# Kernel optimization log

Measured on AMD Instinct MI355X. Metric: run time of the kernel, lower is better.

The kernel has to match this reference:

```python
import jax, jax.numpy as jnp
import numpy as np

N = 50000
HID = 128
NH = 4
E_RES, E_SEQ, E_KNN = 100000, 100000, 200000
BN_EPS = 1e-5
NEG_SLOPE = 0.2


def _gat(h, src, dst, W, al, ar, resW, b):
    """DGL-style GATConv (eval mode: feat_drop off, residual=True, bias).
    h: (N, in), W/resW: (in, H*out), al/ar: (H, out), b: (H*out,)"""
    Hh, out = al.shape
    feat = (h @ W).reshape(N, Hh, out)                 # (N, H, out)
    el = jnp.sum(feat * al, axis=-1)                   # (N, H)
    er = jnp.sum(feat * ar, axis=-1)                   # (N, H)
    e = jax.nn.leaky_relu(el[src] + er[dst], NEG_SLOPE)  # (E, H)
    # edge softmax over incoming edges of each dst node (numerically stable)
    m = jax.ops.segment_max(e, dst, num_segments=N)    # (N, H)
    ex = jnp.exp(e - m[dst])
    s = jax.ops.segment_sum(ex, dst, num_segments=N)
    a = ex / s[dst]                                    # (E, H)
    msg = a[:, :, None] * feat[src]                    # (E, H, out)
    rst = jax.ops.segment_sum(msg, dst, num_segments=N)  # (N, H, out)
    return rst + (h @ resW).reshape(N, Hh, out) + b.reshape(1, Hh, out)


def _hetero(h, src_res, dst_res, src_seq, dst_seq, src_knn, dst_knn, W, al, ar, resW, b):
    # HeteroGraphConv with aggregate='sum' over relations, then mean over heads
    r = _gat(h, src_res, dst_res, W[0], al[0], ar[0], resW[0], b[0])
    r = r + _gat(h, src_seq, dst_seq, W[1], al[1], ar[1], resW[1], b[1])
    r = r + _gat(h, src_knn, dst_knn, W[2], al[2], ar[2], resW[2], b[2])
    return jnp.mean(r, axis=1)                         # (N, out)


def setup_inputs() -> dict:
    key = jax.random.key(0)
    ks = iter(jax.random.split(key, 32))
    inp = {}
    inp["x"] = jax.random.normal(next(ks), (N, HID), jnp.float32)
    inp["src_res"] = jax.random.randint(next(ks), (E_RES,), 0, N, jnp.int32)
    inp["dst_res"] = jax.random.randint(next(ks), (E_RES,), 0, N, jnp.int32)
    inp["src_seq"] = jax.random.randint(next(ks), (E_SEQ,), 0, N, jnp.int32)
    inp["dst_seq"] = jax.random.randint(next(ks), (E_SEQ,), 0, N, jnp.int32)
    inp["src_knn"] = jax.random.randint(next(ks), (E_KNN,), 0, N, jnp.int32)
    inp["dst_knn"] = jax.random.randint(next(ks), (E_KNN,), 0, N, jnp.int32)
    sc = 0.05
    for l in (0, 1):
        inp[f"W{l}"] = jax.random.normal(next(ks), (3, HID, NH * HID), jnp.float32) * sc
        inp[f"al{l}"] = jax.random.normal(next(ks), (3, NH, HID), jnp.float32) * sc
        inp[f"ar{l}"] = jax.random.normal(next(ks), (3, NH, HID), jnp.float32) * sc
        inp[f"resW{l}"] = jax.random.normal(next(ks), (3, HID, NH * HID), jnp.float32) * sc
        inp[f"b{l}"] = jax.random.normal(next(ks), (3, NH * HID), jnp.float32) * sc
    inp["fc_W"] = jax.random.normal(next(ks), (HID, HID), jnp.float32) * sc
    inp["fc_b"] = jax.random.normal(next(ks), (HID,), jnp.float32) * sc
    inp["bn_gamma"] = jnp.ones((HID,), jnp.float32)
    inp["bn_beta"] = jnp.zeros((HID,), jnp.float32)
    inp["bn_mean"] = jax.random.normal(next(ks), (HID,), jnp.float32) * sc
    inp["bn_var"] = jax.random.uniform(next(ks), (HID,), jnp.float32)
    return inp


def reference(x, src_res, dst_res, src_seq, dst_seq, src_knn, dst_knn,
              W0, al0, ar0, resW0, b0, W1, al1, ar1, resW1, b1,
              fc_W, fc_b, bn_gamma, bn_beta, bn_mean, bn_var):
    # layer 0: hetero GAT, head-mean, fc + ReLU + BatchNorm (eval), dropout=identity
    h = _hetero(x, src_res, dst_res, src_seq, dst_seq, src_knn, dst_knn,
                W0, al0, ar0, resW0, b0)
    h = jax.nn.relu(h @ fc_W + fc_b)
    h = (h - bn_mean) / jnp.sqrt(bn_var + BN_EPS) * bn_gamma + bn_beta
    # layer 1 (final): hetero GAT, head-mean
    out = _hetero(h, src_res, dst_res, src_seq, dst_seq, src_knn, dst_knn,
                  W1, al1, ar1, resW1, b1)
    return out
```

## Files before the change

kernel.cpp:

```cpp
#include <hip/hip_runtime.h>
#include <hip/hip_bf16.h>
#include <math.h>
#include <stdint.h>

#define NNODES 50000
#define SCHUNK 4096
#define AW 1664
#define XOFF 1536

typedef __bf16 bf16x8 __attribute__((ext_vector_type(8)));
typedef float f32x4 __attribute__((ext_vector_type(4)));
typedef unsigned short u16;
typedef unsigned int u32;

__device__ __forceinline__ float lrelu(float x){ return x >= 0.f ? x : 0.2f*x; }
__device__ __forceinline__ float b2f(u16 u){ union{ u32 i; float f; } c; c.i = ((u32)u)<<16; return c.f; }
__device__ __forceinline__ float lo2f(u32 v){ union{ u32 i; float f; } c; c.i = v<<16; return c.f; }
__device__ __forceinline__ float hi2f(u32 v){ union{ u32 i; float f; } c; c.i = v & 0xffff0000u; return c.f; }
__device__ __forceinline__ u16 f2b(float f){ __hip_bfloat16 h = __float2bfloat16(f); return *(u16*)&h; }
__device__ __forceinline__ u32 packbf(float a, float b){ return (u32)f2b(a) | ((u32)f2b(b) << 16); }

#define GLDS16(g, l) __builtin_amdgcn_global_load_lds( \
    (const __attribute__((address_space(1))) void*)(g), \
    (__attribute__((address_space(3))) void*)(l), 16, 0, 0)

__global__ void prep_b(const float* __restrict__ W0, const float* __restrict__ W1,
                       const float* __restrict__ resW0, const float* __restrict__ resW1,
                       const float* __restrict__ b0, const float* __restrict__ b1,
                       u16* __restrict__ Btb, float* __restrict__ biasf)
{
    int gid = blockIdx.x*blockDim.x + threadIdx.x;
    if (gid < 2*128*AW){
        int l = gid / (128*AW);
        int rem = gid - l*(128*AW);
        int c = rem / AW;
        int j = rem - c*AW;
        const float* W  = l ? W1 : W0;
        const float* rw = l ? resW1 : resW0;
        float v;
        if (j < XOFF){
            int r = j >> 9, h = (j >> 7) & 3, k = j & 127;
            v = 0.25f * W[(size_t)r*65536 + (size_t)k*512 + h*128 + c];
        } else {
            int k = j - XOFF;
            float s = 0.f;
            for (int r = 0; r < 3; ++r)
                for (int h = 0; h < 4; ++h)
                    s += rw[(size_t)r*65536 + (size_t)k*512 + h*128 + c];
            v = 0.25f * s;
        }
        Btb[gid] = f2b(v);
    }
    if (gid < 256){
        int l = gid >> 7, c = gid & 127;
        const float* bb = l ? b1 : b0;
        float s = 0.f;
        for (int r = 0; r < 3; ++r)
            for (int h = 0; h < 4; ++h)
                s += bb[r*512 + h*128 + c];
        biasf[gid] = 0.25f*s;
    }
}

__global__ void prep_wl(const float* __restrict__ W0, const float* __restrict__ W1,
                        const float* __restrict__ al0, const float* __restrict__ ar0,
                        const float* __restrict__ al1, const float* __restrict__ ar1,
                        const float* __restrict__ fcW,
                        u16* __restrict__ wlb, u16* __restrict__ fcWtb)
{
    int gid = blockIdx.x*blockDim.x + threadIdx.x;
    if (gid < 2*128*128){
        int l = gid >> 14;
        int col = (gid >> 7) & 127;
        int k = gid & 127;
        float v = 0.f;
        if (col < 24){
            int r = col >> 3, lr = (col >> 2) & 1, h = col & 3;
            const float* W = l ? W1 : W0;
            const float* av = l ? (lr ? ar1 : al1) : (lr ? ar0 : al0);
            const float* wrow = W + (size_t)r*65536 + (size_t)k*512 + h*128;
            const float* arow = av + r*512 + h*128;
            for (int cc = 0; cc < 128; ++cc) v += wrow[cc]*arow[cc];
        }
        wlb[gid] = f2b(v);
    }
    if (gid < 128*128){
        int k = gid & 127, n = gid >> 7;
        fcWtb[gid] = f2b(fcW[k*128 + n]);
    }
}

__global__ __launch_bounds__(256) void xprep_kernel(const float* __restrict__ x,
    u16* __restrict__ Ax, const u16* __restrict__ wl, float* __restrict__ el, int M)
{
    __shared__ u16 Xs[64*136];
    __shared__ u16 Ws[32*136];
    const int tid = threadIdx.x;
    const int row0 = blockIdx.x*64;
    #pragma unroll
    for (int p = 0; p < 2; ++p){
        int idx = tid + p*256;
        int c = idx >> 4, kc = (idx & 15)*8;
        float4 v = make_float4(0.f,0.f,0.f,0.f);
        if (c < 24) v = *(const float4*)(wl + c*128 + kc);
        *(float4*)&Ws[c*136 + kc] = v;
    }
    int r = tid >> 2, cq = (tid & 3)*32;
    int grow = row0 + r;
    if (grow < M){
        #pragma unroll
        for (int i = 0; i < 8; ++i){
            float4 v = *(const float4*)(x + (size_t)grow*128 + cq + i*4);
            ushort4 o;
            o.x = f2b(v.x); o.y = f2b(v.y); o.z = f2b(v.z); o.w = f2b(v.w);
            *(ushort4*)(Ax + (size_t)grow*AW + cq + i*4) = o;
            *(ushort4*)&Xs[r*136 + cq + i*4] = o;
        }
    } else {
        ushort4 z; z.x=0; z.y=0; z.z=0; z.w=0;
        #pragma unroll
        for (int i = 0; i < 8; ++i) *(ushort4*)&Xs[r*136 + cq + i*4] = z;
    }
    __syncthreads();
    const int lane = tid & 63, wave = tid >> 6;
    const int r16 = lane & 15, quad = lane >> 4;
    f32x4 acc0 = {}, acc1 = {};
    #pragma unroll
    for (int ks = 0; ks < 4; ++ks){
        int ko = ks*32 + quad*8;
        bf16x8 a  = *(const bf16x8*)&Xs[(wave*16 + r16)*136 + ko];
        bf16x8 b0 = *(const bf16x8*)&Ws[r16*136 + ko];
        bf16x8 b1 = *(const bf16x8*)&Ws[(16 + r16)*136 + ko];
        acc0 = __builtin_amdgcn_mfma_f32_16x16x32_bf16(a, b0, acc0, 0,0,0);
        acc1 = __builtin_amdgcn_mfma_f32_16x16x32_bf16(a, b1, acc1, 0,0,0);
    }
    #pragma unroll
    for (int p = 0; p < 4; ++p){
        int row = row0 + wave*16 + quad*4 + p;
        if (row < M){
            el[(size_t)row*32 + r16] = acc0[p];
            if (r16 < 8) el[(size_t)row*32 + 16 + r16] = acc1[p];
        }
    }
}

__global__ void hist_all(const int* __restrict__ d0, const int* __restrict__ d1,
                         const int* __restrict__ d2, int e0, int e1, int e2,
                         int* __restrict__ cnt)
{
    int g = blockIdx.x*blockDim.x + threadIdx.x;
    if (g >= e0 + e1 + e2) return;
    int rel, idx;
    if (g < e0){ rel = 0; idx = g; }
    else if (g < e0 + e1){ rel = 1; idx = g - e0; }
    else { rel = 2; idx = g - e0 - e1; }
    const int* d = rel == 0 ? d0 : (rel == 1 ? d1 : d2);
    atomicAdd(cnt + (size_t)rel*NNODES + d[idx], 1);
}

__global__ __launch_bounds__(256) void scan_part(const int* __restrict__ cnt_all,
                                                 int* __restrict__ partials, int Nn, int nblk)
{
    int rel = blockIdx.y, blk = blockIdx.x;
    const int* cnt = cnt_all + (size_t)rel*Nn;
    int tid = threadIdx.x;
    int i0 = blk*SCHUNK + tid*16;
    int s = 0;
    #pragma unroll
    for (int k = 0; k < 4; ++k){
        int idx = i0 + k*4;
        if (idx + 3 < Nn){ int4 v = *(const int4*)(cnt + idx); s += v.x+v.y+v.z+v.w; }
        else { for (int j = 0; j < 4; ++j) if (idx+j < Nn) s += cnt[idx+j]; }
    }
    #pragma unroll
    for (int off = 1; off < 64; off <<= 1) s += __shfl_xor(s, off);
    __shared__ int ws[4];
    if ((tid & 63) == 0) ws[tid>>6] = s;
    __syncthreads();
    if (tid == 0) partials[rel*nblk + blk] = ws[0]+ws[1]+ws[2]+ws[3];
}

__global__ __launch_bounds__(256) void scan_write(const int* __restrict__ cnt_all,
                                                  const int* __restrict__ partials,
                                                  int* __restrict__ rp_all, int* __restrict__ cur_all,
                                                  int Nn, int nblk)
{
    int rel = blockIdx.y, blk = blockIdx.x;
    const int* cnt = cnt_all + (size_t)rel*Nn;
    int* rp  = rp_all  + (size_t)rel*(Nn+1);
    int* cur = cur_all + (size_t)rel*Nn;
    int tid = threadIdx.x;
    __shared__ int sOff;
    __shared__ int wsum[4];
    if (tid == 0){
        int o = 0;
        for (int b = 0; b < blk; ++b) o += partials[rel*nblk + b];
        sOff = o;
        if (blk == 0){
            int t = 0;
            for (int b = 0; b < nblk; ++b) t += partials[rel*nblk + b];
            rp[Nn] = t;
        }
    }
    int i0 = blk*SCHUNK + tid*16;
    int v[16];
    int s = 0;
    #pragma unroll
    for (int k = 0; k < 16; ++k){
        int idx = i0 + k;
        v[k] = (idx < Nn) ? cnt[idx] : 0;
        s += v[k];
    }
    int lane = tid & 63;
    int incl = s;
    #pragma unroll
    for (int off = 1; off < 64; off <<= 1){
        int t = __shfl_up(incl, off);
        if (lane >= off) incl += t;
    }
    if (lane == 63) wsum[tid>>6] = incl;
    __syncthreads();
    int woff = 0;
    for (int w = 0; w < (tid>>6); ++w) woff += wsum[w];
    int ex = sOff + woff + incl - s;
    #pragma unroll
    for (int k = 0; k < 16; ++k){
        int idx = i0 + k;
        if (idx < Nn){ rp[idx] = ex; cur[idx] = ex; }
        ex += v[k];
    }
}

__global__ void scatter_all(const int* __restrict__ s0, const int* __restrict__ s1,
                            const int* __restrict__ s2,
                            const int* __restrict__ d0, const int* __restrict__ d1,
                            const int* __restrict__ d2, int e0, int e1, int e2,
                            int* __restrict__ cur, int* __restrict__ colb,
                            int* __restrict__ dste)
{
    int g = blockIdx.x*blockDim.x + threadIdx.x;
    if (g >= e0 + e1 + e2) return;
    int rel, idx, coff;
    if (g < e0){ rel = 0; idx = g; coff = 0; }
    else if (g < e0 + e1){ rel = 1; idx = g - e0; coff = e0; }
    else { rel = 2; idx = g - e0 - e1; coff = e0 + e1; }
    const int* sp = rel == 0 ? s0 : (rel == 1 ? s1 : s2);
    const int* dp = rel == 0 ? d0 : (rel == 1 ? d1 : d2);
    int d = dp[idx];
    int pos = atomicAdd(cur + (size_t)rel*NNODES + d, 1);
    colb[coff + pos] = sp[idx];
    dste[coff + pos] = d;
}

__global__ void wprep(const int* __restrict__ colb, const int* __restrict__ dste,
                      int e0, int e01, int etot,
                      const float* __restrict__ el_all, ushort4* __restrict__ colw)
{
    int j = blockIdx.x*blockDim.x + threadIdx.x;
    if (j >= etot) return;
    int rel = (j < e0) ? 0 : ((j < e01) ? 1 : 2);
    int src = colb[j], dst = dste[j];
    float4 es = *(const float4*)(el_all + (size_t)src*32 + rel*8);
    float4 ed = *(const float4*)(el_all + (size_t)dst*32 + rel*8 + 4);
    ushort4 o;
    o.x = f2b(__expf(lrelu(es.x + ed.x)));
    o.y = f2b(__expf(lrelu(es.y + ed.y)));
    o.z = f2b(__expf(lrelu(es.z + ed.z)));
    o.w = f2b(__expf(lrelu(es.w + ed.w)));
    colw[j] = o;
}

__global__ __launch_bounds__(256) void agg2(const int* __restrict__ rowp_all,
    const int* __restrict__ colb_all, const ushort4* __restrict__ colw_all,
    int e0, int e01,
    const u16* __restrict__ Ax, u16* __restrict__ Abuf, int Nn)
{
    const int rel = blockIdx.y;
    const int tid = threadIdx.x;
    const int lane = tid & 63;
    const int hl = lane & 31;
    const int halfbase = lane & 32;
    const int n = (blockIdx.x*256 + tid) >> 5;
    if (n >= Nn) return;
    const int* rowp = rowp_all + (size_t)rel*(Nn+1);
    const int coff = (rel == 0) ? 0 : ((rel == 1) ? e0 : e01);
    const int* colb = colb_all + coff;
    const ushort4* colw = colw_all + coff;
    u16* op = Abuf + (size_t)n*AW + rel*512 + hl*4;

    int beg = rowp[n], end = rowp[n+1];
    if (beg >= end){
        uint2 z; z.x = 0; z.y = 0;
        #pragma unroll
        for (int h = 0; h < 4; ++h) *(uint2*)(op + h*128) = z;
        return;
    }
    float acc[4][4] = {};
    float us0 = 0.f, us1 = 0.f, us2 = 0.f, us3 = 0.f;
    for (int eb = beg; eb < end; eb += 32){
        int j = eb + hl;
        int s = 0; uint2 w2; w2.x = 0; w2.y = 0;
        if (j < end){
            s = colb[j];
            w2 = *(const uint2*)&colw[j];
        }
        us0 += lo2f(w2.x); us1 += hi2f(w2.x);
        us2 += lo2f(w2.y); us3 += hi2f(w2.y);
        int cnt = min(32, end - eb);
        for (int t = 0; t < cnt; ++t){
            int lsrc = halfbase + t;
            int st = __shfl(s, lsrc);
            u32 wa = (u32)__shfl((int)w2.x, lsrc);
            u32 wb = (u32)__shfl((int)w2.y, lsrc);
            float w0 = lo2f(wa), w1 = hi2f(wa), w2f = lo2f(wb), w3 = hi2f(wb);
            uint2 xv = *(const uint2*)(Ax + (size_t)st*AW + hl*4);
            float x0 = lo2f(xv.x), x1 = hi2f(xv.x), x2 = lo2f(xv.y), x3 = hi2f(xv.y);
            acc[0][0] = fmaf(w0, x0, acc[0][0]); acc[0][1] = fmaf(w0, x1, acc[0][1]);
            acc[0][2] = fmaf(w0, x2, acc[0][2]); acc[0][3] = fmaf(w0, x3, acc[0][3]);
            acc[1][0] = fmaf(w1, x0, acc[1][0]); acc[1][1] = fmaf(w1, x1, acc[1][1]);
            acc[1][2] = fmaf(w1, x2, acc[1][2]); acc[1][3] = fmaf(w1, x3, acc[1][3]);
            acc[2][0] = fmaf(w2f, x0, acc[2][0]); acc[2][1] = fmaf(w2f, x1, acc[2][1]);
            acc[2][2] = fmaf(w2f, x2, acc[2][2]); acc[2][3] = fmaf(w2f, x3, acc[2][3]);
            acc[3][0] = fmaf(w3, x0, acc[3][0]); acc[3][1] = fmaf(w3, x1, acc[3][1]);
            acc[3][2] = fmaf(w3, x2, acc[3][2]); acc[3][3] = fmaf(w3, x3, acc[3][3]);
        }
    }
    #pragma unroll
    for (int off = 1; off < 32; off <<= 1){
        us0 += __shfl_xor(us0, off); us1 += __shfl_xor(us1, off);
        us2 += __shfl_xor(us2, off); us3 += __shfl_xor(us3, off);
    }
    float inv[4] = {1.f/us0, 1.f/us1, 1.f/us2, 1.f/us3};
    #pragma unroll
    for (int h = 0; h < 4; ++h){
        uint2 o;
        o.x = packbf(acc[h][0]*inv[h], acc[h][1]*inv[h]);
        o.y = packbf(acc[h][2]*inv[h], acc[h][3]*inv[h]);
        *(uint2*)(op + h*128) = o;
    }
}

template<int EPI, int ELR>
__global__ __launch_bounds__(256) void gemm_f(
    const u16* __restrict__ A, int Astride, int K,
    const u16* __restrict__ Bt,
    float* __restrict__ Cf, u16* __restrict__ Cb, int Cstride, int M,
    const float* __restrict__ bias, const float* __restrict__ gamma,
    const float* __restrict__ beta, const float* __restrict__ mean,
    const float* __restrict__ var,
    const u16* __restrict__ wl, float* __restrict__ el)
{
    __shared__ u16 smem[24576];
    const int tid = threadIdx.x;
    const int row0 = blockIdx.x*64;
    const int lane = tid & 63, wave = tid >> 6;
    const int wm = (wave >> 1)*32, wn = (wave & 1)*64;
    const int r16 = lane & 15, quad = lane >> 4;
    const int swzbase = r16 & 7;
    f32x4 acc[2][4] = {};

    const int r8 = lane >> 3, jc = lane & 7;
    const int soff = ((jc ^ r8) << 3);
    int gA0 = row0 + wave*16 + r8;      if (gA0 >= M) gA0 = M - 1;
    int gA1 = row0 + wave*16 + 8 + r8;  if (gA1 >= M) gA1 = M - 1;
    const u16* srcA0 = A + (size_t)gA0*Astride + soff;
    const u16* srcA1 = A + (size_t)gA1*Astride + soff;
    const u16* srcB0 = Bt + (size_t)(wave*32      + r8)*K + soff;
    const u16* srcB1 = Bt + (size_t)(wave*32 + 8  + r8)*K + soff;
    const u16* srcB2 = Bt + (size_t)(wave*32 + 16 + r8)*K + soff;
    const u16* srcB3 = Bt + (size_t)(wave*32 + 24 + r8)*K + soff;
    const int nk = K >> 6;

    #define STAGE(buf, k0) do { \
        u16* As_ = smem + (buf)*12288; \
        u16* Bs_ = As_ + 4096; \
        GLDS16(srcA0 + (k0), As_ + wave*1024); \
        GLDS16(srcA1 + (k0), As_ + wave*1024 + 512); \
        GLDS16(srcB0 + (k0), Bs_ + wave*2048); \
        GLDS16(srcB1 + (k0), Bs_ + wave*2048 + 512); \
        GLDS16(srcB2 + (k0), Bs_ + wave*2048 + 1024); \
        GLDS16(srcB3 + (k0), Bs_ + wave*2048 + 1536); \
    } while (0)

    STAGE(0, 0);
    __syncthreads();
    for (int t = 0; t < nk; ++t){
        int cur = t & 1;
        if (t + 1 < nk) STAGE(cur ^ 1, (t + 1) << 6);
        const u16* As = smem + cur*12288;
        const u16* Bs = As + 4096;
        #pragma unroll
        for (int ks = 0; ks < 2; ++ks){
            int swz = ((ks*4 + quad) ^ swzbase) << 3;
            bf16x8 a0 = *(const bf16x8*)&As[(wm + r16)*64 + swz];
            bf16x8 a1 = *(const bf16x8*)&As[(wm + 16 + r16)*64 + swz];
            #pragma unroll
            for (int j = 0; j < 4; ++j){
                bf16x8 b = *(const bf16x8*)&Bs[(wn + j*16 + r16)*64 + swz];
                acc[0][j] = __builtin_amdgcn_mfma_f32_16x16x32_bf16(a0, b, acc[0][j], 0,0,0);
                acc[1][j] = __builtin_amdgcn_mfma_f32_16x16x32_bf16(a1, b, acc[1][j], 0,0,0);
            }
        }
        __syncthreads();
    }
    #undef STAGE

    u16* Cs = smem;
    u16* Ws = smem + 64*136;
    if (ELR){
        #pragma unroll
        for (int p = 0; p < 2; ++p){
            int idx = tid + p*256;
            int c = idx >> 4, kc = (idx & 15)*8;
            float4 v = make_float4(0.f,0.f,0.f,0.f);
            if (c < 24) v = *(const float4*)(wl + c*128 + kc);
            *(float4*)&Ws[c*136 + kc] = v;
        }
    }
    #pragma unroll
    for (int i = 0; i < 2; ++i){
        #pragma unroll
        for (int p = 0; p < 4; ++p){
            int rl = wm + i*16 + quad*4 + p;
            int row = row0 + rl;
            #pragma unroll
            for (int j = 0; j < 4; ++j){
                int col = wn + j*16 + r16;
                float v = acc[i][j][p] + bias[col];
                if (EPI == 2){
                    float t = fmaxf(v, 0.f);
                    v = (t - mean[col]) * rsqrtf(var[col] + 1e-5f) * gamma[col] + beta[col];
                }
                u16 vb = f2b(v);
                if (row < M){
                    if (EPI == 1) Cf[(size_t)row*Cstride + col] = v;
                    else          Cb[(size_t)row*Cstride + col] = vb;
                }
                if (ELR) Cs[rl*136 + col] = vb;
            }
        }
    }
    if (ELR){
        __syncthreads();
        f32x4 e0 = {}, e1 = {};
        #pragma unroll
        for (int ks = 0; ks < 4; ++ks){
            int ko = ks*32 + quad*8;
            bf16x8 a  = *(const bf16x8*)&Cs[(wave*16 + r16)*136 + ko];
            bf16x8 b0 = *(const bf16x8*)&Ws[r16*136 + ko];
            bf16x8 b1 = *(const bf16x8*)&Ws[(16 + r16)*136 + ko];
            e0 = __builtin_amdgcn_mfma_f32_16x16x32_bf16(a, b0, e0, 0,0,0);
            e1 = __builtin_amdgcn_mfma_f32_16x16x32_bf16(a, b1, e1, 0,0,0);
        }
        #pragma unroll
        for (int p = 0; p < 4; ++p){
            int row = row0 + wave*16 + quad*4 + p;
            if (row < M){
                el[(size_t)row*32 + r16] = e0[p];
                if (r16 < 8) el[(size_t)row*32 + 16 + r16] = e1[p];
            }
        }
    }
}

static inline char* align256(char* p){ return (char*)(((uintptr_t)p + 255) & ~(uintptr_t)255); }

extern "C" void kernel_launch(void* const* d_in, const int* in_sizes, int n_in,
                              void* d_out, int out_size, void* d_ws, size_t ws_size,
                              hipStream_t stream)
{
    const float* x      = (const float*)d_in[0];
    const int* srcs[3]  = {(const int*)d_in[1], (const int*)d_in[3], (const int*)d_in[5]};
    const int* dsts[3]  = {(const int*)d_in[2], (const int*)d_in[4], (const int*)d_in[6]};
    const int  E[3]     = {in_sizes[1], in_sizes[3], in_sizes[5]};
    const float* W0     = (const float*)d_in[7];
    const float* al0    = (const float*)d_in[8];
    const float* ar0    = (const float*)d_in[9];
    const float* resW0  = (const float*)d_in[10];
    const float* b0     = (const float*)d_in[11];
    const float* W1     = (const float*)d_in[12];
    const float* al1    = (const float*)d_in[13];
    const float* ar1    = (const float*)d_in[14];
    const float* resW1  = (const float*)d_in[15];
    const float* b1     = (const float*)d_in[16];
    const float* fcW    = (const float*)d_in[17];
    const float* fcb    = (const float*)d_in[18];
    const float* gamma  = (const float*)d_in[19];
    const float* beta   = (const float*)d_in[20];
    const float* bmean  = (const float*)d_in[21];
    const float* bvar   = (const float*)d_in[22];
    float* out = (float*)d_out;

    char* p = (char*)d_ws;
    u16*   Abuf  = (u16*)p;   p += (size_t)NNODES*AW*2;    p = align256(p);
    float* el    = (float*)p; p += (size_t)NNODES*32*4;    p = align256(p);
    u16*   hmb   = (u16*)p;   p += (size_t)NNODES*128*2;   p = align256(p);
    int*   cnt   = (int*)p;   p += (size_t)3*NNODES*4;     p = align256(p);
    int*   rowp  = (int*)p;   p += (size_t)3*(NNODES+1)*4; p = align256(p);
    int*   cur   = (int*)p;   p += (size_t)3*NNODES*4;     p = align256(p);
    int*   colb  = (int*)p;   p += (size_t)(E[0]+E[1]+E[2])*4; p = align256(p);
    int*   dste  = (int*)p;   p += (size_t)(E[0]+E[1]+E[2])*4; p = align256(p);
    ushort4* colw= (ushort4*)p; p += (size_t)(E[0]+E[1]+E[2])*8; p = align256(p);
    u16*   Btb   = (u16*)p;   p += (size_t)2*128*AW*2;     p = align256(p);
    u16*   wlb   = (u16*)p;   p += (size_t)2*128*128*2;    p = align256(p);
    u16*   fcWtb = (u16*)p;   p += (size_t)128*128*2;      p = align256(p);
    float* biasf = (float*)p; p += (size_t)2*128*4;        p = align256(p);
    int*   parts = (int*)p;   p += (size_t)3*64*4;

    const int NBLK = (NNODES + SCHUNK - 1)/SCHUNK;
    const int MB = (NNODES + 63)/64;
    const int AGGBLKS = (NNODES + 7)/8;
    const int ETOT = E[0] + E[1] + E[2];
    dim3 blk(256);
    u16* Ax = Abuf + XOFF;

    hipMemsetAsync(cnt, 0, (size_t)3*NNODES*sizeof(int), stream);
    prep_b <<<(2*128*AW + 255)/256, blk, 0, stream>>>(W0, W1, resW0, resW1, b0, b1, Btb, biasf);
    prep_wl<<<(2*128*128 + 255)/256, blk, 0, stream>>>(W0, W1, al0, ar0, al1, ar1, fcW, wlb, fcWtb);
    xprep_kernel<<<MB, blk, 0, stream>>>(x, Ax, wlb, el, NNODES);
    hist_all<<<(ETOT + 255)/256, blk, 0, stream>>>(dsts[0], dsts[1], dsts[2], E[0], E[1], E[2], cnt);
    scan_part <<<dim3(NBLK,3), blk, 0, stream>>>(cnt, parts, NNODES, NBLK);
    scan_write<<<dim3(NBLK,3), blk, 0, stream>>>(cnt, parts, rowp, cur, NNODES, NBLK);
    scatter_all<<<(ETOT + 255)/256, blk, 0, stream>>>(srcs[0], srcs[1], srcs[2],
                                                      dsts[0], dsts[1], dsts[2],
                                                      E[0], E[1], E[2], cur, colb, dste);

    wprep<<<(ETOT + 255)/256, blk, 0, stream>>>(colb, dste, E[0], E[0]+E[1], ETOT, el, colw);
    agg2<<<dim3(AGGBLKS,3), blk, 0, stream>>>(rowp, colb, colw, E[0], E[0]+E[1], Ax, Abuf, NNODES);
    gemm_f<4,0><<<MB, blk, 0, stream>>>(Abuf, AW, AW, Btb, nullptr, hmb, 128, NNODES,
                                        biasf, nullptr, nullptr, nullptr, nullptr, nullptr, nullptr);
    gemm_f<2,1><<<MB, blk, 0, stream>>>(hmb, 128, 128, fcWtb, nullptr, Ax, AW, NNODES,
                                        fcb, gamma, beta, bmean, bvar, wlb + 16384, el);

    wprep<<<(ETOT + 255)/256, blk, 0, stream>>>(colb, dste, E[0], E[0]+E[1], ETOT, el, colw);
    agg2<<<dim3(AGGBLKS,3), blk, 0, stream>>>(rowp, colb, colw, E[0], E[0]+E[1], Ax, Abuf, NNODES);
    gemm_f<1,0><<<MB, blk, 0, stream>>>(Abuf, AW, AW, Btb + (size_t)128*AW, out, nullptr, 128, NNODES,
                                        biasf + 128, nullptr, nullptr, nullptr, nullptr, nullptr, nullptr);
}
```

Baseline: 392.5 us.

## Pack edge src and weights into 16-byte records and prefetch in aggregation

The edge-prep kernel now writes one 16-byte record per edge holding the source index and the packed bf16 softmax numerators, in place of separate index and weight arrays. The aggregation kernel switches from 32 lanes per node with shuffle broadcasts to 16 lanes per node, each loading 8 features with 16-byte loads. Each thread walks its node's edges sequentially with a two-deep software prefetch of records and gathered rows. This removes shuffles and widens memory accesses, but doubles per-edge record bandwidth and uses more accumulator registers.

Measured after the change: 390.0 us. No clear change (-0.6%).

```diff
diff --git a/kernel.cpp b/kernel.cpp
--- a/kernel.cpp
+++ b/kernel.cpp
@@ -254,7 +254,7 @@
 
 __global__ void wprep(const int* __restrict__ colb, const int* __restrict__ dste,
                       int e0, int e01, int etot,
-                      const float* __restrict__ el_all, ushort4* __restrict__ colw)
+                      const float* __restrict__ el_all, uint4* __restrict__ rec)
 {
     int j = blockIdx.x*blockDim.x + threadIdx.x;
     if (j >= etot) return;
@@ -262,81 +262,76 @@
     int src = colb[j], dst = dste[j];
     float4 es = *(const float4*)(el_all + (size_t)src*32 + rel*8);
     float4 ed = *(const float4*)(el_all + (size_t)dst*32 + rel*8 + 4);
-    ushort4 o;
-    o.x = f2b(__expf(lrelu(es.x + ed.x)));
-    o.y = f2b(__expf(lrelu(es.y + ed.y)));
-    o.z = f2b(__expf(lrelu(es.z + ed.z)));
-    o.w = f2b(__expf(lrelu(es.w + ed.w)));
-    colw[j] = o;
-}
-
-__global__ __launch_bounds__(256) void agg2(const int* __restrict__ rowp_all,
-    const int* __restrict__ colb_all, const ushort4* __restrict__ colw_all,
-    int e0, int e01,
+    uint4 o;
+    o.x = (u32)src;
+    o.y = packbf(__expf(lrelu(es.x + ed.x)), __expf(lrelu(es.y + ed.y)));
+    o.z = packbf(__expf(lrelu(es.z + ed.z)), __expf(lrelu(es.w + ed.w)));
+    o.w = 0;
+    rec[j] = o;
+}
+
+__global__ __launch_bounds__(256) void agg3(const int* __restrict__ rowp_all,
+    const uint4* __restrict__ rec_all, int e0, int e01,
     const u16* __restrict__ Ax, u16* __restrict__ Abuf, int Nn)
 {
     const int rel = blockIdx.y;
     const int tid = threadIdx.x;
-    const int lane = tid & 63;
-    const int hl = lane & 31;
-    const int halfbase = lane & 32;
-    const int n = (blockIdx.x*256 + tid) >> 5;
+    const int o = tid & 15;
+    const int n = (blockIdx.x*256 + tid) >> 4;
     if (n >= Nn) return;
     const int* rowp = rowp_all + (size_t)rel*(Nn+1);
     const int coff = (rel == 0) ? 0 : ((rel == 1) ? e0 : e01);
-    const int* colb = colb_all + coff;
-    const ushort4* colw = colw_all + coff;
-    u16* op = Abuf + (size_t)n*AW + rel*512 + hl*4;
+    const uint4* rec = rec_all + coff;
+    u16* op = Abuf + (size_t)n*AW + rel*512 + o*8;
 
     int beg = rowp[n], end = rowp[n+1];
     if (beg >= end){
-        uint2 z; z.x = 0; z.y = 0;
-        #pragma unroll
-        for (int h = 0; h < 4; ++h) *(uint2*)(op + h*128) = z;
+        uint4 z; z.x = 0; z.y = 0; z.z = 0; z.w = 0;
+        #pragma unroll
+        for (int h = 0; h < 4; ++h) *(uint4*)(op + h*128) = z;
         return;
     }
-    float acc[4][4] = {};
+    float acc[4][8] = {};
     float us0 = 0.f, us1 = 0.f, us2 = 0.f, us3 = 0.f;
-    for (int eb = beg; eb < end; eb += 32){
-        int j = eb + hl;
-        int s = 0; uint2 w2; w2.x = 0; w2.y = 0;
-        if (j < end){
-            s = colb[j];
-            w2 = *(const uint2*)&colw[j];
-        }
-        us0 += lo2f(w2.x); us1 += hi2f(w2.x);
-        us2 += lo2f(w2.y); us3 += hi2f(w2.y);
-        int cnt = min(32, end - eb);
-        for (int t = 0; t < cnt; ++t){
-            int lsrc = halfbase + t;
-            int st = __shfl(s, lsrc);
-            u32 wa = (u32)__shfl((int)w2.x, lsrc);
-            u32 wb = (u32)__shfl((int)w2.y, lsrc);
-            float w0 = lo2f(wa), w1 = hi2f(wa), w2f = lo2f(wb), w3 = hi2f(wb);
-            uint2 xv = *(const uint2*)(Ax + (size_t)st*AW + hl*4);
-            float x0 = lo2f(xv.x), x1 = hi2f(xv.x), x2 = lo2f(xv.y), x3 = hi2f(xv.y);
-            acc[0][0] = fmaf(w0, x0, acc[0][0]); acc[0][1] = fmaf(w0, x1, acc[0][1]);
-            acc[0][2] = fmaf(w0, x2, acc[0][2]); acc[0][3] = fmaf(w0, x3, acc[0][3]);
-            acc[1][0] = fmaf(w1, x0, acc[1][0]); acc[1][1] = fmaf(w1, x1, acc[1][1]);
-            acc[1][2] = fmaf(w1, x2, acc[1][2]); acc[1][3] = fmaf(w1, x3, acc[1][3]);
-            acc[2][0] = fmaf(w2f, x0, acc[2][0]); acc[2][1] = fmaf(w2f, x1, acc[2][1]);
-            acc[2][2] = fmaf(w2f, x2, acc[2][2]); acc[2][3] = fmaf(w2f, x3, acc[2][3]);
-            acc[3][0] = fmaf(w3, x0, acc[3][0]); acc[3][1] = fmaf(w3, x1, acc[3][1]);
-            acc[3][2] = fmaf(w3, x2, acc[3][2]); acc[3][3] = fmaf(w3, x3, acc[3][3]);
-        }
-    }
-    #pragma unroll
-    for (int off = 1; off < 32; off <<= 1){
-        us0 += __shfl_xor(us0, off); us1 += __shfl_xor(us1, off);
-        us2 += __shfl_xor(us2, off); us3 += __shfl_xor(us3, off);
+
+    uint4 ra = rec[beg];
+    uint4 xa = *(const uint4*)(Ax + (size_t)ra.x*AW + o*8);
+    uint4 rb = ra, xb = xa;
+    if (beg + 1 < end){
+        rb = rec[beg+1];
+        xb = *(const uint4*)(Ax + (size_t)rb.x*AW + o*8);
+    }
+    for (int j = beg; j < end; ++j){
+        uint4 rc = rb, xc = xb;
+        if (j + 2 < end){
+            rc = rec[j+2];
+            xc = *(const uint4*)(Ax + (size_t)rc.x*AW + o*8);
+        }
+        float w0 = lo2f(ra.y), w1 = hi2f(ra.y), w2 = lo2f(ra.z), w3 = hi2f(ra.z);
+        us0 += w0; us1 += w1; us2 += w2; us3 += w3;
+        float xv[8];
+        xv[0] = lo2f(xa.x); xv[1] = hi2f(xa.x);
+        xv[2] = lo2f(xa.y); xv[3] = hi2f(xa.y);
+        xv[4] = lo2f(xa.z); xv[5] = hi2f(xa.z);
+        xv[6] = lo2f(xa.w); xv[7] = hi2f(xa.w);
+        #pragma unroll
+        for (int c = 0; c < 8; ++c){
+            acc[0][c] = fmaf(w0, xv[c], acc[0][c]);
+            acc[1][c] = fmaf(w1, xv[c], acc[1][c]);
+            acc[2][c] = fmaf(w2, xv[c], acc[2][c]);
+            acc[3][c] = fmaf(w3, xv[c], acc[3][c]);
+        }
+        ra = rb; xa = xb; rb = rc; xb = xc;
     }
     float inv[4] = {1.f/us0, 1.f/us1, 1.f/us2, 1.f/us3};
     #pragma unroll
     for (int h = 0; h < 4; ++h){
-        uint2 o;
-        o.x = packbf(acc[h][0]*inv[h], acc[h][1]*inv[h]);
-        o.y = packbf(acc[h][2]*inv[h], acc[h][3]*inv[h]);
-        *(uint2*)(op + h*128) = o;
+        uint4 ov;
+        ov.x = packbf(acc[h][0]*inv[h], acc[h][1]*inv[h]);
+        ov.y = packbf(acc[h][2]*inv[h], acc[h][3]*inv[h]);
+        ov.z = packbf(acc[h][4]*inv[h], acc[h][5]*inv[h]);
+        ov.w = packbf(acc[h][6]*inv[h], acc[h][7]*inv[h]);
+        *(uint4*)(op + h*128) = ov;
     }
 }
 
@@ -500,7 +495,7 @@
     int*   cur   = (int*)p;   p += (size_t)3*NNODES*4;     p = align256(p);
     int*   colb  = (int*)p;   p += (size_t)(E[0]+E[1]+E[2])*4; p = align256(p);
     int*   dste  = (int*)p;   p += (size_t)(E[0]+E[1]+E[2])*4; p = align256(p);
-    ushort4* colw= (ushort4*)p; p += (size_t)(E[0]+E[1]+E[2])*8; p = align256(p);
+    uint4* rec   = (uint4*)p; p += (size_t)(E[0]+E[1]+E[2])*16; p = align256(p);
     u16*   Btb   = (u16*)p;   p += (size_t)2*128*AW*2;     p = align256(p);
     u16*   wlb   = (u16*)p;   p += (size_t)2*128*128*2;    p = align256(p);
     u16*   fcWtb = (u16*)p;   p += (size_t)128*128*2;      p = align256(p);
@@ -509,7 +504,7 @@
 
     const int NBLK = (NNODES + SCHUNK - 1)/SCHUNK;
     const int MB = (NNODES + 63)/64;
-    const int AGGBLKS = (NNODES + 7)/8;
+    const int AGGBLKS = (NNODES*16 + 255)/256;
     const int ETOT = E[0] + E[1] + E[2];
     dim3 blk(256);
     u16* Ax = Abuf + XOFF;
@@ -525,15 +520,15 @@
                                                       dsts[0], dsts[1], dsts[2],
                                                       E[0], E[1], E[2], cur, colb, dste);
 
-    wprep<<<(ETOT + 255)/256, blk, 0, stream>>>(colb, dste, E[0], E[0]+E[1], ETOT, el, colw);
-    agg2<<<dim3(AGGBLKS,3), blk, 0, stream>>>(rowp, colb, colw, E[0], E[0]+E[1], Ax, Abuf, NNODES);
+    wprep<<<(ETOT + 255)/256, blk, 0, stream>>>(colb, dste, E[0], E[0]+E[1], ETOT, el, rec);
+    agg3<<<dim3(AGGBLKS,3), blk, 0, stream>>>(rowp, rec, E[0], E[0]+E[1], Ax, Abuf, NNODES);
     gemm_f<4,0><<<MB, blk, 0, stream>>>(Abuf, AW, AW, Btb, nullptr, hmb, 128, NNODES,
                                         biasf, nullptr, nullptr, nullptr, nullptr, nullptr, nullptr);
     gemm_f<2,1><<<MB, blk, 0, stream>>>(hmb, 128, 128, fcWtb, nullptr, Ax, AW, NNODES,
                                         fcb, gamma, beta, bmean, bvar, wlb + 16384, el);
 
-    wprep<<<(ETOT + 255)/256, blk, 0, stream>>>(colb, dste, E[0], E[0]+E[1], ETOT, el, colw);
-    agg2<<<dim3(AGGBLKS,3), blk, 0, stream>>>(rowp, colb, colw, E[0], E[0]+E[1], Ax, Abuf, NNODES);
+    wprep<<<(ETOT + 255)/256, blk, 0, stream>>>(colb, dste, E[0], E[0]+E[1], ETOT, el, rec);
+    agg3<<<dim3(AGGBLKS,3), blk, 0, stream>>>(rowp, rec, E[0], E[0]+E[1], Ax, Abuf, NNODES);
     gemm_f<1,0><<<MB, blk, 0, stream>>>(Abuf, AW, AW, Btb + (size_t)128*AW, out, nullptr, 128, NNODES,
                                         biasf + 128, nullptr, nullptr, nullptr, nullptr, nullptr, nullptr);
 }
```
